# Performance work log

Hardware: AMD Instinct MI355X
Metric: run time of the kernel (lower is better)

The kernel has to match this reference:

```python
import jax, jax.numpy as jnp
import numpy as np

INF = 10000000000.0
D_KEY = 512
SCALE = np.sqrt(D_KEY).astype(np.float32)

def setup_inputs() -> dict:
    key = jax.random.key(0)
    kq, kk, kv = jax.random.split(key, 3)
    B, S, D = 16, 2048, D_KEY
    return {
        "query": jax.random.normal(kq, (B, S, D), dtype=jnp.float32),
        "key": jax.random.normal(kk, (B, S, D), dtype=jnp.float32),
        "value": jax.random.normal(kv, (B, S, D), dtype=jnp.float32),
    }

def reference(query, key, value):
    # dot_products = Q @ K^T, shape [B, S, S]
    scores = jnp.einsum('bqd,bkd->bqk', query, key)
    S = key.shape[1]
    # causal mask: subtract INF on strict upper triangle (applied BEFORE scaling,
    # matching the original which subtracts tri*INF then divides by scale)
    tri = jnp.triu(jnp.ones((S, S), dtype=scores.dtype), k=1) * INF
    scores = scores - tri[None, :, :]
    attn = jax.nn.softmax(scores / SCALE, axis=-1)
    return jnp.einsum('bqk,bkd->bqd', attn, value)
```

## Files before the change

### kernel.cpp

```cpp
#include <hip/hip_runtime.h>

typedef float  f32x4 __attribute__((ext_vector_type(4)));
typedef short  s16x8 __attribute__((ext_vector_type(8)));
typedef short  s16x4 __attribute__((ext_vector_type(4)));

#define B_   16
#define S_   2048
#define D_   512
#define BM   32
#define BN   256
#define RSCALE 0.04419417382415922f
#define LOG2E  1.4426950408889634f

__device__ __forceinline__ short f2bf(float f){
    unsigned u = __float_as_uint(f);
    u += 0x7fffu + ((u >> 16) & 1u);
    return (short)(u >> 16);
}

__device__ __forceinline__ f32x4 max4(f32x4 a, f32x4 b){
    f32x4 r; r[0]=fmaxf(a[0],b[0]); r[1]=fmaxf(a[1],b[1]);
             r[2]=fmaxf(a[2],b[2]); r[3]=fmaxf(a[3],b[3]); return r;
}
__device__ __forceinline__ f32x4 shfl_xor4(f32x4 v, int mask){
    f32x4 r; r[0]=__shfl_xor(v[0],mask); r[1]=__shfl_xor(v[1],mask);
             r[2]=__shfl_xor(v[2],mask); r[3]=__shfl_xor(v[3],mask); return r;
}

__global__ void cast_k_kernel(const float* __restrict__ k, short* __restrict__ kb){
    const long n4 = (long)B_*S_*D_/4;
    const float4* src = (const float4*)k;
    for (long t = (long)blockIdx.x*blockDim.x + threadIdx.x; t < n4;
         t += (long)gridDim.x*blockDim.x){
        float4 v = src[t];
        s16x4 o; o[0]=f2bf(v.x); o[1]=f2bf(v.y); o[2]=f2bf(v.z); o[3]=f2bf(v.w);
        *(s16x4*)(kb + t*4) = o;
    }
}

__global__ void transpose_v_kernel(const float* __restrict__ v, short* __restrict__ vt){
    __shared__ float tile[64][65];
    int b  = blockIdx.z;
    int s0 = blockIdx.x * 64;
    int d0 = blockIdx.y * 64;
    int t  = threadIdx.x;
    int r  = t >> 2;
    int c4 = (t & 3) * 16;
    const float* src = v + ((long)b*S_ + s0 + r)*D_ + d0 + c4;
    float4 a0 = ((const float4*)src)[0];
    float4 a1 = ((const float4*)src)[1];
    float4 a2 = ((const float4*)src)[2];
    float4 a3 = ((const float4*)src)[3];
    tile[r][c4+ 0]=a0.x; tile[r][c4+ 1]=a0.y; tile[r][c4+ 2]=a0.z; tile[r][c4+ 3]=a0.w;
    tile[r][c4+ 4]=a1.x; tile[r][c4+ 5]=a1.y; tile[r][c4+ 6]=a1.z; tile[r][c4+ 7]=a1.w;
    tile[r][c4+ 8]=a2.x; tile[r][c4+ 9]=a2.y; tile[r][c4+10]=a2.z; tile[r][c4+11]=a2.w;
    tile[r][c4+12]=a3.x; tile[r][c4+13]=a3.y; tile[r][c4+14]=a3.z; tile[r][c4+15]=a3.w;
    __syncthreads();
    s16x8 w0, w1;
    #pragma unroll
    for (int i = 0; i < 8; ++i)  w0[i] = f2bf(tile[c4+i][r]);
    #pragma unroll
    for (int i = 0; i < 8; ++i)  w1[i] = f2bf(tile[c4+8+i][r]);
    short* dst = vt + ((long)b*D_ + d0 + r)*S_ + s0 + c4;
    *(s16x8*)dst       = w0;
    *(s16x8*)(dst + 8) = w1;
}

__global__ __launch_bounds__(512) void flash_kernel(
    const float* __restrict__ q, const short* __restrict__ kb,
    const short* __restrict__ vt, float* __restrict__ out)
{
    __shared__ __align__(16) short q_lds[BM*D_];
    __shared__ __align__(16) short p_lds[BM*BN];
    __shared__ float pmax[BM][8];
    __shared__ float psum[BM][8];

    int bx = blockIdx.x;
    int lo = bx & 7;
    int hi = bx >> 3;
    int batch = 2*lo + (hi & 1);
    int t = hi >> 1;
    int qt = (t < 32) ? (63 - t) : (t - 32);
    int q0 = qt * BM;

    int tid  = threadIdx.x;
    int w    = tid >> 6;
    int lane = tid & 63;
    int m    = lane & 15;
    int quad = lane >> 4;

    {
        int r  = tid >> 4;
        int cb = (tid & 15) << 5;
        const float* qrow = q + ((long)batch*S_ + q0 + r)*D_;
        #pragma unroll
        for (int gi = 0; gi < 4; ++gi){
            int c = cb + gi*8;
            float4 f0 = *(const float4*)(qrow + c);
            float4 f1 = *(const float4*)(qrow + c + 4);
            s16x8 vv;
            vv[0]=f2bf(f0.x); vv[1]=f2bf(f0.y); vv[2]=f2bf(f0.z); vv[3]=f2bf(f0.w);
            vv[4]=f2bf(f1.x); vv[5]=f2bf(f1.y); vv[6]=f2bf(f1.z); vv[7]=f2bf(f1.w);
            int g = c >> 3;
            *(s16x8*)&q_lds[r*D_ + (((g ^ (r & 7)) & 63) << 3)] = vv;
        }
    }
    __syncthreads();

    f32x4 o_acc[2][4];
    #pragma unroll
    for (int a = 0; a < 2; ++a)
        #pragma unroll
        for (int b2 = 0; b2 < 4; ++b2) o_acc[a][b2] = (f32x4)0.0f;
    f32x4 m_pr[2], l_pr[2];
    m_pr[0] = (f32x4)(-1e30f); m_pr[1] = (f32x4)(-1e30f);
    l_pr[0] = (f32x4)0.0f;     l_pr[1] = (f32x4)0.0f;

    const short* kbb = kb + (long)batch*S_*D_;
    const short* vtb = vt + (long)batch*D_*S_;
    int jmax = (q0 + BM - 1) >> 8;

    for (int j = 0; j <= jmax; ++j){
        int kbase = j << 8;

        f32x4 acc[2][2];
        acc[0][0]=(f32x4)0.0f; acc[0][1]=(f32x4)0.0f;
        acc[1][0]=(f32x4)0.0f; acc[1][1]=(f32x4)0.0f;
        const short* kp0 = kbb + ((long)(kbase + w*32 + m))*D_ + quad*8;
        #pragma unroll
        for (int ks = 0; ks < 16; ++ks){
            int gq = ((ks*4 + quad) ^ (m & 7)) << 3;
            s16x8 a0 = *(const s16x8*)&q_lds[ m      *D_ + gq];
            s16x8 a1 = *(const s16x8*)&q_lds[(16 + m)*D_ + gq];
            const short* kp = kp0 + ks*32;
            s16x8 b0 = *(const s16x8*)kp;
            s16x8 b1 = *(const s16x8*)(kp + 16*D_);
            acc[0][0] = __builtin_amdgcn_mfma_f32_16x16x32_bf16(a0, b0, acc[0][0], 0,0,0);
            acc[0][1] = __builtin_amdgcn_mfma_f32_16x16x32_bf16(a0, b1, acc[0][1], 0,0,0);
            acc[1][0] = __builtin_amdgcn_mfma_f32_16x16x32_bf16(a1, b0, acc[1][0], 0,0,0);
            acc[1][1] = __builtin_amdgcn_mfma_f32_16x16x32_bf16(a1, b1, acc[1][1], 0,0,0);
        }

        if (j == jmax){
            #pragma unroll
            for (int mt = 0; mt < 2; ++mt)
                #pragma unroll
                for (int nt = 0; nt < 2; ++nt){
                    int kg = kbase + w*32 + nt*16 + m;
                    #pragma unroll
                    for (int rr = 0; rr < 4; ++rr){
                        int qg = q0 + mt*16 + quad*4 + rr;
                        float vv = acc[mt][nt][rr] * RSCALE;
                        acc[mt][nt][rr] = (kg > qg) ? -1e30f : vv;
                    }
                }
        } else {
            #pragma unroll
            for (int mt = 0; mt < 2; ++mt)
                #pragma unroll
                for (int nt = 0; nt < 2; ++nt)
                    #pragma unroll
                    for (int rr = 0; rr < 4; ++rr)
                        acc[mt][nt][rr] *= RSCALE;
        }

        f32x4 cm[2];
        cm[0] = max4(acc[0][0], acc[0][1]);
        cm[1] = max4(acc[1][0], acc[1][1]);
        #pragma unroll
        for (int msk = 1; msk < 16; msk <<= 1){
            cm[0] = max4(cm[0], shfl_xor4(cm[0], msk));
            cm[1] = max4(cm[1], shfl_xor4(cm[1], msk));
        }
        if (m == 0){
            #pragma unroll
            for (int mt = 0; mt < 2; ++mt)
                #pragma unroll
                for (int rr = 0; rr < 4; ++rr)
                    pmax[mt*16 + quad*4 + rr][w] = cm[mt][rr];
        }
        __syncthreads();

        f32x4 alpha[2];
        #pragma unroll
        for (int mt = 0; mt < 2; ++mt){
            #pragma unroll
            for (int rr = 0; rr < 4; ++rr){
                int row = mt*16 + quad*4 + rr;
                f32x4 p0 = *(const f32x4*)&pmax[row][0];
                f32x4 p1 = *(const f32x4*)&pmax[row][4];
                f32x4 pm = max4(p0, p1);
                float mx = fmaxf(fmaxf(pm[0],pm[1]), fmaxf(pm[2],pm[3]));
                float mn = fmaxf(m_pr[mt][rr], mx);
                alpha[mt][rr] = exp2f((m_pr[mt][rr] - mn) * LOG2E);
                m_pr[mt][rr] = mn;
            }
            l_pr[mt] *= alpha[mt];
            #pragma unroll
            for (int nt = 0; nt < 4; ++nt) o_acc[mt][nt] *= alpha[mt];
        }

        f32x4 cs[2]; cs[0] = (f32x4)0.0f; cs[1] = (f32x4)0.0f;
        #pragma unroll
        for (int mt = 0; mt < 2; ++mt)
            #pragma unroll
            for (int nt = 0; nt < 2; ++nt){
                int col = w*32 + nt*16 + m;
                int g   = col >> 3;
                #pragma unroll
                for (int rr = 0; rr < 4; ++rr){
                    int row = mt*16 + quad*4 + rr;
                    float p = exp2f((acc[mt][nt][rr] - m_pr[mt][rr]) * LOG2E);
                    cs[mt][rr] += p;
                    p_lds[row*BN + (((g ^ (row & 7)) & 31) << 3) + (col & 7)] = f2bf(p);
                }
            }
        #pragma unroll
        for (int msk = 1; msk < 16; msk <<= 1){
            cs[0] = cs[0] + shfl_xor4(cs[0], msk);
            cs[1] = cs[1] + shfl_xor4(cs[1], msk);
        }
        if (m == 0){
            #pragma unroll
            for (int mt = 0; mt < 2; ++mt)
                #pragma unroll
                for (int rr = 0; rr < 4; ++rr)
                    psum[mt*16 + quad*4 + rr][w] = cs[mt][rr];
        }
        __syncthreads();

        #pragma unroll
        for (int mt = 0; mt < 2; ++mt)
            #pragma unroll
            for (int rr = 0; rr < 4; ++rr){
                int row = mt*16 + quad*4 + rr;
                f32x4 p0 = *(const f32x4*)&psum[row][0];
                f32x4 p1 = *(const f32x4*)&psum[row][4];
                f32x4 sm = p0 + p1;
                l_pr[mt][rr] += (sm[0]+sm[1]) + (sm[2]+sm[3]);
            }

        const short* vp0 = vtb + ((long)(w*64 + m))*S_ + kbase + quad*8;
        #pragma unroll
        for (int ks = 0; ks < 8; ++ks){
            int gp = ((ks*4 + quad) ^ (m & 7)) << 3;
            s16x8 pa0 = *(const s16x8*)&p_lds[ m      *BN + gp];
            s16x8 pa1 = *(const s16x8*)&p_lds[(16 + m)*BN + gp];
            const short* vp = vp0 + ks*32;
            s16x8 vb0 = *(const s16x8*)vp;
            s16x8 vb1 = *(const s16x8*)(vp + 16*S_);
            s16x8 vb2 = *(const s16x8*)(vp + 32*S_);
            s16x8 vb3 = *(const s16x8*)(vp + 48*S_);
            o_acc[0][0] = __builtin_amdgcn_mfma_f32_16x16x32_bf16(pa0, vb0, o_acc[0][0], 0,0,0);
            o_acc[0][1] = __builtin_amdgcn_mfma_f32_16x16x32_bf16(pa0, vb1, o_acc[0][1], 0,0,0);
            o_acc[0][2] = __builtin_amdgcn_mfma_f32_16x16x32_bf16(pa0, vb2, o_acc[0][2], 0,0,0);
            o_acc[0][3] = __builtin_amdgcn_mfma_f32_16x16x32_bf16(pa0, vb3, o_acc[0][3], 0,0,0);
            o_acc[1][0] = __builtin_amdgcn_mfma_f32_16x16x32_bf16(pa1, vb0, o_acc[1][0], 0,0,0);
            o_acc[1][1] = __builtin_amdgcn_mfma_f32_16x16x32_bf16(pa1, vb1, o_acc[1][1], 0,0,0);
            o_acc[1][2] = __builtin_amdgcn_mfma_f32_16x16x32_bf16(pa1, vb2, o_acc[1][2], 0,0,0);
            o_acc[1][3] = __builtin_amdgcn_mfma_f32_16x16x32_bf16(pa1, vb3, o_acc[1][3], 0,0,0);
        }
    }

    float* ob = out + ((long)batch*S_ + q0)*D_ + w*64;
    #pragma unroll
    for (int mt = 0; mt < 2; ++mt){
        f32x4 inv;
        #pragma unroll
        for (int rr = 0; rr < 4; ++rr) inv[rr] = 1.0f / l_pr[mt][rr];
        #pragma unroll
        for (int nt = 0; nt < 4; ++nt){
            f32x4 vv = o_acc[mt][nt] * inv;
            #pragma unroll
            for (int rr = 0; rr < 4; ++rr)
                ob[(long)(mt*16 + quad*4 + rr)*D_ + nt*16 + m] = vv[rr];
        }
    }
}

extern "C" void kernel_launch(void* const* d_in, const int* in_sizes, int n_in,
                              void* d_out, int out_size, void* d_ws, size_t ws_size,
                              hipStream_t stream) {
    const float* q = (const float*)d_in[0];
    const float* k = (const float*)d_in[1];
    const float* v = (const float*)d_in[2];
    float* out = (float*)d_out;
    short* kbb = (short*)d_ws;
    short* vtb = kbb + (size_t)B_*S_*D_;
    cast_k_kernel<<<8192, 256, 0, stream>>>(k, kbb);
    transpose_v_kernel<<<dim3(S_/64, D_/64, B_), 256, 0, stream>>>(v, vtb);
    flash_kernel<<<1024, 512, 0, stream>>>(q, kbb, vtb, out);
}
```

Measured before the change: 525.5 us.

## Software-pipeline K and V global loads into registers across flash-attention stages

Adds register prefetch rings for K fragments (depth 3) and V fragments (double buffered), so global loads for upcoming MFMA steps are issued before the current step's MFMAs. V loads for a tile are started before the softmax phase, and the next tile's first K fragments are loaded before the PV loop. It also raises wave priority around the MFMA loops with s_setprio and adds a min-waves hint to launch_bounds. The aim is to hide global-load latency behind compute, at the cost of more vector registers, which could force spills under the occupancy hint.

```diff
diff --git a/kernel.cpp b/kernel.cpp
--- a/kernel.cpp
+++ b/kernel.cpp
@@ -9,6 +9,7 @@
 #define D_   512
 #define BM   32
 #define BN   256
+#define KPF  3
 #define RSCALE 0.04419417382415922f
 #define LOG2E  1.4426950408889634f
 
@@ -66,7 +67,7 @@
     *(s16x8*)(dst + 8) = w1;
 }
 
-__global__ __launch_bounds__(512) void flash_kernel(
+__global__ __launch_bounds__(512, 4) void flash_kernel(
     const float* __restrict__ q, const short* __restrict__ kb,
     const short* __restrict__ vt, float* __restrict__ out)
 {
@@ -120,26 +121,50 @@
     const short* vtb = vt + (long)batch*D_*S_;
     int jmax = (q0 + BM - 1) >> 8;
 
+    s16x8 kr0[KPF], kr1[KPF];
+    {
+        const short* kp = kbb + ((long)(w*32 + m))*D_ + quad*8;
+        #pragma unroll
+        for (int pf = 0; pf < KPF; ++pf){
+            kr0[pf] = *(const s16x8*)(kp + pf*32);
+            kr1[pf] = *(const s16x8*)(kp + pf*32 + 16*D_);
+        }
+    }
+
     for (int j = 0; j <= jmax; ++j){
         int kbase = j << 8;
+        const short* kp0 = kbb + ((long)(kbase + w*32 + m))*D_ + quad*8;
 
         f32x4 acc[2][2];
         acc[0][0]=(f32x4)0.0f; acc[0][1]=(f32x4)0.0f;
         acc[1][0]=(f32x4)0.0f; acc[1][1]=(f32x4)0.0f;
-        const short* kp0 = kbb + ((long)(kbase + w*32 + m))*D_ + quad*8;
+        __builtin_amdgcn_s_setprio(1);
         #pragma unroll
         for (int ks = 0; ks < 16; ++ks){
+            const int sl = ks % KPF;
+            s16x8 b0 = kr0[sl];
+            s16x8 b1 = kr1[sl];
+            if (ks + KPF < 16){
+                const short* kp = kp0 + (ks + KPF)*32;
+                kr0[sl] = *(const s16x8*)kp;
+                kr1[sl] = *(const s16x8*)(kp + 16*D_);
+            }
             int gq = ((ks*4 + quad) ^ (m & 7)) << 3;
             s16x8 a0 = *(const s16x8*)&q_lds[ m      *D_ + gq];
             s16x8 a1 = *(const s16x8*)&q_lds[(16 + m)*D_ + gq];
-            const short* kp = kp0 + ks*32;
-            s16x8 b0 = *(const s16x8*)kp;
-            s16x8 b1 = *(const s16x8*)(kp + 16*D_);
             acc[0][0] = __builtin_amdgcn_mfma_f32_16x16x32_bf16(a0, b0, acc[0][0], 0,0,0);
             acc[0][1] = __builtin_amdgcn_mfma_f32_16x16x32_bf16(a0, b1, acc[0][1], 0,0,0);
             acc[1][0] = __builtin_amdgcn_mfma_f32_16x16x32_bf16(a1, b0, acc[1][0], 0,0,0);
             acc[1][1] = __builtin_amdgcn_mfma_f32_16x16x32_bf16(a1, b1, acc[1][1], 0,0,0);
         }
+        __builtin_amdgcn_s_setprio(0);
+
+        const short* vp0 = vtb + ((long)(w*64 + m))*S_ + kbase + quad*8;
+        s16x8 vA[4], vB[4];
+        #pragma unroll
+        for (int g = 0; g < 4; ++g) vA[g] = *(const s16x8*)(vp0 + g*16*S_);
+        #pragma unroll
+        for (int g = 0; g < 4; ++g) vB[g] = *(const s16x8*)(vp0 + 32 + g*16*S_);
 
         if (j == jmax){
             #pragma unroll
@@ -240,17 +265,34 @@
                 l_pr[mt][rr] += (sm[0]+sm[1]) + (sm[2]+sm[3]);
             }
 
-        const short* vp0 = vtb + ((long)(w*64 + m))*S_ + kbase + quad*8;
+        if (j < jmax){
+            const short* kp = kbb + ((long)(kbase + 256 + w*32 + m))*D_ + quad*8;
+            #pragma unroll
+            for (int pf = 0; pf < KPF; ++pf){
+                kr0[pf] = *(const s16x8*)(kp + pf*32);
+                kr1[pf] = *(const s16x8*)(kp + pf*32 + 16*D_);
+            }
+        }
+
+        __builtin_amdgcn_s_setprio(1);
         #pragma unroll
         for (int ks = 0; ks < 8; ++ks){
+            s16x8 vb0, vb1, vb2, vb3;
+            if (ks & 1){ vb0=vB[0]; vb1=vB[1]; vb2=vB[2]; vb3=vB[3]; }
+            else       { vb0=vA[0]; vb1=vA[1]; vb2=vA[2]; vb3=vA[3]; }
+            if (ks + 2 < 8){
+                const short* vp = vp0 + (ks+2)*32;
+                if (ks & 1){
+                    #pragma unroll
+                    for (int g = 0; g < 4; ++g) vB[g] = *(const s16x8*)(vp + g*16*S_);
+                } else {
+                    #pragma unroll
+                    for (int g = 0; g < 4; ++g) vA[g] = *(const s16x8*)(vp + g*16*S_);
+                }
+            }
             int gp = ((ks*4 + quad) ^ (m & 7)) << 3;
             s16x8 pa0 = *(const s16x8*)&p_lds[ m      *BN + gp];
             s16x8 pa1 = *(const s16x8*)&p_lds[(16 + m)*BN + gp];
-            const short* vp = vp0 + ks*32;
-            s16x8 vb0 = *(const s16x8*)vp;
-            s16x8 vb1 = *(const s16x8*)(vp + 16*S_);
-            s16x8 vb2 = *(const s16x8*)(vp + 32*S_);
-            s16x8 vb3 = *(const s16x8*)(vp + 48*S_);
             o_acc[0][0] = __builtin_amdgcn_mfma_f32_16x16x32_bf16(pa0, vb0, o_acc[0][0], 0,0,0);
             o_acc[0][1] = __builtin_amdgcn_mfma_f32_16x16x32_bf16(pa0, vb1, o_acc[0][1], 0,0,0);
             o_acc[0][2] = __builtin_amdgcn_mfma_f32_16x16x32_bf16(pa0, vb2, o_acc[0][2], 0,0,0);
@@ -260,6 +302,7 @@
             o_acc[1][2] = __builtin_amdgcn_mfma_f32_16x16x32_bf16(pa1, vb2, o_acc[1][2], 0,0,0);
             o_acc[1][3] = __builtin_amdgcn_mfma_f32_16x16x32_bf16(pa1, vb3, o_acc[1][3], 0,0,0);
         }
+        __builtin_amdgcn_s_setprio(0);
     }
 
     float* ob = out + ((long)batch*S_ + q0)*D_ + w*64;
```

Result: slower. 841.5 us (+60.1%).
